# Kernel optimization log

Measured on AMD Instinct MI355X. Metric: run time of the kernel, lower is better.

The kernel has to match this reference:

```python
import jax, jax.numpy as jnp
import numpy as np

GRID = 385  # (W+1) = (H+1) = (D+1) corners of a 384^3 voxel grid


def setup_inputs() -> dict:
    key = jax.random.key(0)
    occ = jax.random.uniform(key, (GRID, GRID, GRID), dtype=jnp.float32)
    return {"occ": occ}


def reference(occ):
    # Occupancy connectivity loss: sum over axis-aligned neighbor pairs of
    # |occ_i - occ_j| (each pair counted once via the 3 forward directions).
    lx = jnp.sum(jnp.abs(occ[1:, :, :] - occ[:-1, :, :]))
    ly = jnp.sum(jnp.abs(occ[:, 1:, :] - occ[:, :-1, :]))
    lz = jnp.sum(jnp.abs(occ[:, :, 1:] - occ[:, :, :-1]))
    return lx + ly + lz
```

## Files before the change

kernel.cpp:

```cpp
#include <hip/hip_runtime.h>


constexpr int          G     = 385;
constexpr int          PLANE = G * G;
constexpr long long    NTOT  = (long long)G * PLANE;
constexpr int          N4    = (int)((NTOT + 3) / 4);

#define TPB    256
#define BLOCKS 2048

__global__ __launch_bounds__(TPB) void occ_conn_partial(
    const float* __restrict__ a, float* __restrict__ ws)
{
    float s = 0.f;
    const int stride = BLOCKS * TPB;
    for (int i = blockIdx.x * TPB + threadIdx.x; i < N4; i += stride) {
        const long long p0 = (long long)i * 4;
        if (p0 + 4 < NTOT) {
            const float4 v4 = *(const float4*)(a + p0);
            const float v[4] = {v4.x, v4.y, v4.z, v4.w};
            const float vnext = a[p0 + 4];
            #pragma unroll
            for (int e = 0; e < 4; ++e) {
                const unsigned p = (unsigned)p0 + (unsigned)e;
                const unsigned x = p / (unsigned)PLANE;
                const unsigned r = p - x * (unsigned)PLANE;
                const unsigned y = r / (unsigned)G;
                const unsigned z = r - y * (unsigned)G;
                const float v0 = v[e];
                if (z < (unsigned)(G - 1)) {
                    const float zn = (e < 3) ? v[e + 1] : vnext;
                    s += fabsf(zn - v0);
                }
                if (y < (unsigned)(G - 1)) s += fabsf(a[p + G] - v0);
                if (x < (unsigned)(G - 1)) s += fabsf(a[p + PLANE] - v0);
            }
        } else {
            #pragma unroll
            for (int e = 0; e < 4; ++e) {
                const long long pl = p0 + e;
                if (pl >= NTOT) break;
                const unsigned p = (unsigned)pl;
                const unsigned x = p / (unsigned)PLANE;
                const unsigned r = p - x * (unsigned)PLANE;
                const unsigned y = r / (unsigned)G;
                const unsigned z = r - y * (unsigned)G;
                const float v0 = a[p];
                if (z < (unsigned)(G - 1)) s += fabsf(a[p + 1]     - v0);
                if (y < (unsigned)(G - 1)) s += fabsf(a[p + G]     - v0);
                if (x < (unsigned)(G - 1)) s += fabsf(a[p + PLANE] - v0);
            }
        }
    }

    #pragma unroll
    for (int off = 32; off > 0; off >>= 1) s += __shfl_down(s, off, 64);

    __shared__ float ls[TPB / 64];
    const int lane = threadIdx.x & 63;
    const int wid  = threadIdx.x >> 6;
    if (lane == 0) ls[wid] = s;
    __syncthreads();
    if (threadIdx.x == 0) {
        float t = 0.f;
        #pragma unroll
        for (int w = 0; w < TPB / 64; ++w) t += ls[w];
        ws[blockIdx.x] = t;
    }
}

__global__ __launch_bounds__(256) void occ_conn_final(
    const float* __restrict__ ws, float* __restrict__ out)
{
    float s = 0.f;
    for (int i = threadIdx.x; i < BLOCKS; i += 256) s += ws[i];
    #pragma unroll
    for (int off = 32; off > 0; off >>= 1) s += __shfl_down(s, off, 64);
    __shared__ float ls[4];
    const int lane = threadIdx.x & 63;
    const int wid  = threadIdx.x >> 6;
    if (lane == 0) ls[wid] = s;
    __syncthreads();
    if (threadIdx.x == 0) out[0] = ls[0] + ls[1] + ls[2] + ls[3];
}

extern "C" void kernel_launch(void* const* d_in, const int* in_sizes, int n_in,
                              void* d_out, int out_size, void* d_ws, size_t ws_size,
                              hipStream_t stream)
{
    const float* a   = (const float*)d_in[0];
    float*       out = (float*)d_out;
    float*       ws  = (float*)d_ws;

    occ_conn_partial<<<BLOCKS, TPB, 0, stream>>>(a, ws);
    occ_conn_final<<<1, 256, 0, stream>>>(ws, out);
}
```

Before: 373.8 us.

## Compute all neighbor diffs unconditionally and subtract boundary wrap terms separately

The main pass now computes the z, y and x differences for every element of the first 384 x-planes without per-element index division or boundary branches. It processes 8 elements per thread with vector loads, and the work is split into 8 slabs. A separate set of fixup blocks subtracts the spurious wrap-around terms at row and plane boundaries and handles the last x-plane. This removes the integer divides and divergent branches from the hot loop. In exchange, the result now relies on boundary terms cancelling exactly, so float rounding may differ slightly, and the y/x neighbor loads are unaligned.

```diff
diff --git a/kernel.cpp b/kernel.cpp
--- a/kernel.cpp
+++ b/kernel.cpp
@@ -1,55 +1,79 @@
 #include <hip/hip_runtime.h>
 
 
-constexpr int          G     = 385;
-constexpr int          PLANE = G * G;
-constexpr long long    NTOT  = (long long)G * PLANE;
-constexpr int          N4    = (int)((NTOT + 3) / 4);
+constexpr int      G      = 385;
+constexpr int      PLANE  = G * G;
+constexpr unsigned NTOT   = 57066625u;
+constexpr unsigned NA     = 384u * PLANE;
+constexpr unsigned SLAB   = NA / 8;
+constexpr unsigned SLAB8  = SLAB / 8;
+constexpr unsigned NROWB  = 147840u;
+constexpr unsigned NYB    = 147840u;
 
-#define TPB    256
-#define BLOCKS 2048
+#define TPB        256
+#define FIX_BLOCKS 64
+#define SUB_BLOCKS 248
+#define MAIN_BLOCKS (SUB_BLOCKS * 8)
+#define ALL_BLOCKS  (FIX_BLOCKS + MAIN_BLOCKS)
 
-__global__ __launch_bounds__(TPB) void occ_conn_partial(
+typedef float f4v __attribute__((ext_vector_type(4)));
+typedef f4v f4u __attribute__((aligned(4)));
+
+static __device__ __forceinline__ f4v ld4a(const float* p) { return *(const f4v*)p; }
+static __device__ __forceinline__ f4v ld4u(const float* p) { return *(const f4u*)p; }
+
+__global__ __launch_bounds__(TPB) void occ_conn_main(
     const float* __restrict__ a, float* __restrict__ ws)
 {
     float s = 0.f;
-    const int stride = BLOCKS * TPB;
-    for (int i = blockIdx.x * TPB + threadIdx.x; i < N4; i += stride) {
-        const long long p0 = (long long)i * 4;
-        if (p0 + 4 < NTOT) {
-            const float4 v4 = *(const float4*)(a + p0);
-            const float v[4] = {v4.x, v4.y, v4.z, v4.w};
-            const float vnext = a[p0 + 4];
-            #pragma unroll
-            for (int e = 0; e < 4; ++e) {
-                const unsigned p = (unsigned)p0 + (unsigned)e;
-                const unsigned x = p / (unsigned)PLANE;
-                const unsigned r = p - x * (unsigned)PLANE;
-                const unsigned y = r / (unsigned)G;
-                const unsigned z = r - y * (unsigned)G;
-                const float v0 = v[e];
-                if (z < (unsigned)(G - 1)) {
-                    const float zn = (e < 3) ? v[e + 1] : vnext;
-                    s += fabsf(zn - v0);
-                }
-                if (y < (unsigned)(G - 1)) s += fabsf(a[p + G] - v0);
-                if (x < (unsigned)(G - 1)) s += fabsf(a[p + PLANE] - v0);
-            }
-        } else {
-            #pragma unroll
-            for (int e = 0; e < 4; ++e) {
-                const long long pl = p0 + e;
-                if (pl >= NTOT) break;
-                const unsigned p = (unsigned)pl;
-                const unsigned x = p / (unsigned)PLANE;
-                const unsigned r = p - x * (unsigned)PLANE;
-                const unsigned y = r / (unsigned)G;
-                const unsigned z = r - y * (unsigned)G;
-                const float v0 = a[p];
-                if (z < (unsigned)(G - 1)) s += fabsf(a[p + 1]     - v0);
-                if (y < (unsigned)(G - 1)) s += fabsf(a[p + G]     - v0);
-                if (x < (unsigned)(G - 1)) s += fabsf(a[p + PLANE] - v0);
-            }
+    const int bid = blockIdx.x;
+
+    if (bid < FIX_BLOCKS) {
+        const unsigned ft = (unsigned)bid * TPB + threadIdx.x;
+        const unsigned NF = FIX_BLOCKS * TPB;
+
+        for (unsigned r = ft; r < NROWB; r += NF) {
+            const unsigned p = r * (unsigned)G + 384u;
+            s -= fabsf(a[p + 1] - a[p]);
+        }
+        for (unsigned j = ft; j < NYB; j += NF) {
+            const unsigned x = j / (unsigned)G;
+            const unsigned z = j - x * (unsigned)G;
+            const unsigned q = x * (unsigned)PLANE + 384u * (unsigned)G + z;
+            s -= fabsf(a[q + G] - a[q]);
+        }
+        for (unsigned j = ft; j < (unsigned)PLANE; j += NF) {
+            const unsigned y = j / (unsigned)G;
+            const unsigned z = j - y * (unsigned)G;
+            const unsigned p = NA + j;
+            if (z < 384u) s += fabsf(a[p + 1] - a[p]);
+            if (y < 384u) s += fabsf(a[p + G] - a[p]);
+        }
+    } else {
+        const int mid  = bid - FIX_BLOCKS;
+        const unsigned slab = (unsigned)(mid & 7);
+        const unsigned sub  = (unsigned)(mid >> 3);
+        const unsigned base = slab * SLAB;
+
+        for (unsigned it = sub * TPB + threadIdx.x; it < SLAB8; it += SUB_BLOCKS * TPB) {
+            const unsigned p = base + it * 8u;
+            const f4v f0 = ld4a(a + p);
+            const f4v f1 = ld4a(a + p + 4);
+            const f4v g0 = ld4u(a + p + G);
+            const f4v g1 = ld4u(a + p + G + 4);
+            const f4v h0 = ld4u(a + p + PLANE);
+            const f4v h1 = ld4u(a + p + PLANE + 4);
+            const float fn = a[p + 8];
+
+            s += fabsf(f0.y - f0.x) + fabsf(f0.z - f0.y) + fabsf(f0.w - f0.z)
+               + fabsf(f1.x - f0.w) + fabsf(f1.y - f1.x) + fabsf(f1.z - f1.y)
+               + fabsf(f1.w - f1.z) + fabsf(fn   - f1.w);
+            s += fabsf(g0.x - f0.x) + fabsf(g0.y - f0.y) + fabsf(g0.z - f0.z)
+               + fabsf(g0.w - f0.w) + fabsf(g1.x - f1.x) + fabsf(g1.y - f1.y)
+               + fabsf(g1.z - f1.z) + fabsf(g1.w - f1.w);
+            s += fabsf(h0.x - f0.x) + fabsf(h0.y - f0.y) + fabsf(h0.z - f0.z)
+               + fabsf(h0.w - f0.w) + fabsf(h1.x - f1.x) + fabsf(h1.y - f1.y)
+               + fabsf(h1.z - f1.z) + fabsf(h1.w - f1.w);
         }
     }
 
@@ -73,7 +97,7 @@
     const float* __restrict__ ws, float* __restrict__ out)
 {
     float s = 0.f;
-    for (int i = threadIdx.x; i < BLOCKS; i += 256) s += ws[i];
+    for (int i = threadIdx.x; i < ALL_BLOCKS; i += 256) s += ws[i];
     #pragma unroll
     for (int off = 32; off > 0; off >>= 1) s += __shfl_down(s, off, 64);
     __shared__ float ls[4];
@@ -92,6 +116,6 @@
     float*       out = (float*)d_out;
     float*       ws  = (float*)d_ws;
 
-    occ_conn_partial<<<BLOCKS, TPB, 0, stream>>>(a, ws);
+    occ_conn_main<<<ALL_BLOCKS, TPB, 0, stream>>>(a, ws);
     occ_conn_final<<<1, 256, 0, stream>>>(ws, out);
 }
```

Measured after the change: 325.4 us. -12.9%, faster.

## Tile grid into z-y slabs marching along x with shared-memory halo reuse

Applied to the files above, without the earlier changes.

Replaces the flat grid-stride loop, which did per-element div/mod and three scattered global loads, with 2D tiles (16 y-rows by 64 z-columns) that march along x. Each plane slice is staged in double-buffered LDS with a halo, and the x-neighbor difference is taken from registers holding the previous plane. The y=384 and z=384 boundary faces are handled by eight separate fixup blocks. The aim is to read each element from DRAM roughly once and drop the index arithmetic, at the cost of one __syncthreads per plane, 4-byte-aligned unaligned vector loads, and more intricate boundary handling.

```diff
diff --git a/kernel.cpp b/kernel.cpp
--- a/kernel.cpp
+++ b/kernel.cpp
@@ -1,55 +1,96 @@
 #include <hip/hip_runtime.h>
 
 
-constexpr int          G     = 385;
-constexpr int          PLANE = G * G;
-constexpr long long    NTOT  = (long long)G * PLANE;
-constexpr int          N4    = (int)((NTOT + 3) / 4);
+constexpr int G     = 385;
+constexpr int PLANE = G * G;
+constexpr int ZT = 6, YT = 24, XC = 16;
+constexpr int XP = 384 / XC;
 
-#define TPB    256
-#define BLOCKS 2048
+#define TPB   256
+#define FIXB  8
+#define TILES (ZT * YT * XC)
+#define ALLB  (TILES + FIXB)
 
-__global__ __launch_bounds__(TPB) void occ_conn_partial(
+typedef float f4v __attribute__((ext_vector_type(4)));
+typedef f4v f4u __attribute__((aligned(4)));
+static __device__ __forceinline__ f4v ld4(const float* p) { return *(const f4u*)p; }
+
+__global__ __launch_bounds__(TPB) void occ_conn_main(
     const float* __restrict__ a, float* __restrict__ ws)
 {
     float s = 0.f;
-    const int stride = BLOCKS * TPB;
-    for (int i = blockIdx.x * TPB + threadIdx.x; i < N4; i += stride) {
-        const long long p0 = (long long)i * 4;
-        if (p0 + 4 < NTOT) {
-            const float4 v4 = *(const float4*)(a + p0);
-            const float v[4] = {v4.x, v4.y, v4.z, v4.w};
-            const float vnext = a[p0 + 4];
-            #pragma unroll
-            for (int e = 0; e < 4; ++e) {
-                const unsigned p = (unsigned)p0 + (unsigned)e;
-                const unsigned x = p / (unsigned)PLANE;
-                const unsigned r = p - x * (unsigned)PLANE;
-                const unsigned y = r / (unsigned)G;
-                const unsigned z = r - y * (unsigned)G;
-                const float v0 = v[e];
-                if (z < (unsigned)(G - 1)) {
-                    const float zn = (e < 3) ? v[e + 1] : vnext;
-                    s += fabsf(zn - v0);
-                }
-                if (y < (unsigned)(G - 1)) s += fabsf(a[p + G] - v0);
-                if (x < (unsigned)(G - 1)) s += fabsf(a[p + PLANE] - v0);
+    const int bid = blockIdx.x;
+
+    __shared__ float T[2][17][68];
+
+    if (bid < FIXB) {
+        const unsigned ft = (unsigned)bid * TPB + threadIdx.x;
+        const unsigned NF = FIXB * TPB;
+
+        for (unsigned j = ft; j < 385u * 384u; j += NF) {
+            const unsigned x = j / 384u, z = j - x * 384u;
+            const unsigned p = x * (unsigned)PLANE + 384u * (unsigned)G + z;
+            s += fabsf(a[p + 1] - a[p]);
+        }
+        for (unsigned j = ft; j < 385u * 384u; j += NF) {
+            const unsigned x = j / 384u, y = j - x * 384u;
+            const unsigned p = x * (unsigned)PLANE + y * (unsigned)G + 384u;
+            s += fabsf(a[p + G] - a[p]);
+        }
+        for (unsigned j = ft; j < 384u * 385u; j += NF) {
+            const unsigned x = j / 385u, z = j - x * 385u;
+            const unsigned p = x * (unsigned)PLANE + 384u * (unsigned)G + z;
+            s += fabsf(a[p + PLANE] - a[p]);
+        }
+        for (unsigned j = ft; j < 384u * 384u; j += NF) {
+            const unsigned x = j / 384u, y = j - x * 384u;
+            const unsigned p = x * (unsigned)PLANE + y * (unsigned)G + 384u;
+            s += fabsf(a[p + PLANE] - a[p]);
+        }
+    } else {
+        int t = bid - FIXB;
+        const int bc = t & (XC - 1); t >>= 4;
+        const int by = t % YT;
+        const int bz = t / YT;
+        const int tz = threadIdx.x & 15;
+        const int ty = threadIdx.x >> 4;
+        const int P0 = bc * XP, P1 = P0 + XP;
+        const bool last = (bc == XC - 1);
+
+        const float* pm  = a + (size_t)P0 * PLANE + (size_t)(by * 16 + ty) * G + (bz * 64 + tz * 4);
+        const float* ph  = a + (size_t)P0 * PLANE + (size_t)(by * 16 + 16) * G + (bz * 64 + tz * 4);
+        const float* pc  = a + (size_t)P0 * PLANE + (size_t)(by * 16 + tz) * G + (bz * 64 + 64);
+        const float* pc2 = a + (size_t)P0 * PLANE + (size_t)(by * 16 + 16) * G + (bz * 64 + 64);
+
+        f4v prev;
+        for (int x = P0; x <= P1; ++x) {
+            const int par = x & 1;
+            const f4v cur = ld4(pm);
+            *(f4v*)&T[par][ty][tz * 4] = cur;
+            if (ty == 0)             *(f4v*)&T[par][16][tz * 4] = ld4(ph);
+            if (ty == 1)             T[par][tz][64] = *pc;
+            if (ty == 2 && tz == 0)  T[par][16][64] = *pc2;
+            __syncthreads();
+
+            if (x < P1 || last) {
+                const float v0 = T[par][ty][tz * 4 + 0];
+                const float v1 = T[par][ty][tz * 4 + 1];
+                const float v2 = T[par][ty][tz * 4 + 2];
+                const float v3 = T[par][ty][tz * 4 + 3];
+                const float v4 = T[par][ty][tz * 4 + 4];
+                const float u0 = T[par][ty + 1][tz * 4 + 0];
+                const float u1 = T[par][ty + 1][tz * 4 + 1];
+                const float u2 = T[par][ty + 1][tz * 4 + 2];
+                const float u3 = T[par][ty + 1][tz * 4 + 3];
+                s += fabsf(v1 - v0) + fabsf(v2 - v1) + fabsf(v3 - v2) + fabsf(v4 - v3);
+                s += fabsf(u0 - v0) + fabsf(u1 - v1) + fabsf(u2 - v2) + fabsf(u3 - v3);
             }
-        } else {
-            #pragma unroll
-            for (int e = 0; e < 4; ++e) {
-                const long long pl = p0 + e;
-                if (pl >= NTOT) break;
-                const unsigned p = (unsigned)pl;
-                const unsigned x = p / (unsigned)PLANE;
-                const unsigned r = p - x * (unsigned)PLANE;
-                const unsigned y = r / (unsigned)G;
-                const unsigned z = r - y * (unsigned)G;
-                const float v0 = a[p];
-                if (z < (unsigned)(G - 1)) s += fabsf(a[p + 1]     - v0);
-                if (y < (unsigned)(G - 1)) s += fabsf(a[p + G]     - v0);
-                if (x < (unsigned)(G - 1)) s += fabsf(a[p + PLANE] - v0);
+            if (x > P0) {
+                s += fabsf(cur.x - prev.x) + fabsf(cur.y - prev.y)
+                   + fabsf(cur.z - prev.z) + fabsf(cur.w - prev.w);
             }
+            prev = cur;
+            pm += PLANE; ph += PLANE; pc += PLANE; pc2 += PLANE;
         }
     }
 
@@ -62,10 +103,10 @@
     if (lane == 0) ls[wid] = s;
     __syncthreads();
     if (threadIdx.x == 0) {
-        float t = 0.f;
+        float tsum = 0.f;
         #pragma unroll
-        for (int w = 0; w < TPB / 64; ++w) t += ls[w];
-        ws[blockIdx.x] = t;
+        for (int w = 0; w < TPB / 64; ++w) tsum += ls[w];
+        ws[blockIdx.x] = tsum;
     }
 }
 
@@ -73,7 +114,7 @@
     const float* __restrict__ ws, float* __restrict__ out)
 {
     float s = 0.f;
-    for (int i = threadIdx.x; i < BLOCKS; i += 256) s += ws[i];
+    for (int i = threadIdx.x; i < ALLB; i += 256) s += ws[i];
     #pragma unroll
     for (int off = 32; off > 0; off >>= 1) s += __shfl_down(s, off, 64);
     __shared__ float ls[4];
@@ -92,6 +133,6 @@
     float*       out = (float*)d_out;
     float*       ws  = (float*)d_ws;
 
-    occ_conn_partial<<<BLOCKS, TPB, 0, stream>>>(a, ws);
+    occ_conn_main<<<ALLB, TPB, 0, stream>>>(a, ws);
     occ_conn_final<<<1, 256, 0, stream>>>(ws, out);
 }
```

After: 402.8 us. +7.8%, slower.

## Tile grid into 3D blocks staged in double-buffered shared memory

Applied to the files above, without the earlier changes.

Replaces the flat grid-stride loop, which reloaded y and x neighbours from global memory for every element, with a 3D tiling. Each block covers a 128z by 32y tile and walks 6 x-planes (plus one halo plane), staging each plane plus its halo in double-buffered LDS with aligned float4 loads. The x-neighbour difference comes from the previous plane's buffer, so each element is read from HBM roughly once. Edge cases are handled per tile, which adds control-flow complexity and some halo reloads across x-chunks.

```diff
diff --git a/kernel.cpp b/kernel.cpp
--- a/kernel.cpp
+++ b/kernel.cpp
@@ -1,71 +1,145 @@
 #include <hip/hip_runtime.h>
 
 
-constexpr int          G     = 385;
-constexpr int          PLANE = G * G;
-constexpr long long    NTOT  = (long long)G * PLANE;
-constexpr int          N4    = (int)((NTOT + 3) / 4);
+constexpr int G     = 385;
+constexpr int PLANE = G * G;
 
-#define TPB    256
-#define BLOCKS 2048
+#define TPB  256
+#define ZT   3
+#define YT   12
+#define XC   64
+#define NBLK (ZT * YT * XC)
+#define S    148
 
-__global__ __launch_bounds__(TPB) void occ_conn_partial(
+typedef float f4v __attribute__((ext_vector_type(4)));
+static __device__ __forceinline__ f4v ld4(const float* p) { return *(const f4v*)p; }
+
+__global__ __launch_bounds__(TPB) void occ_conn_main(
     const float* __restrict__ a, float* __restrict__ ws)
 {
+    __shared__ float T[2][33][S];
     float s = 0.f;
-    const int stride = BLOCKS * TPB;
-    for (int i = blockIdx.x * TPB + threadIdx.x; i < N4; i += stride) {
-        const long long p0 = (long long)i * 4;
-        if (p0 + 4 < NTOT) {
-            const float4 v4 = *(const float4*)(a + p0);
-            const float v[4] = {v4.x, v4.y, v4.z, v4.w};
-            const float vnext = a[p0 + 4];
-            #pragma unroll
-            for (int e = 0; e < 4; ++e) {
-                const unsigned p = (unsigned)p0 + (unsigned)e;
-                const unsigned x = p / (unsigned)PLANE;
-                const unsigned r = p - x * (unsigned)PLANE;
-                const unsigned y = r / (unsigned)G;
-                const unsigned z = r - y * (unsigned)G;
-                const float v0 = v[e];
-                if (z < (unsigned)(G - 1)) {
-                    const float zn = (e < 3) ? v[e + 1] : vnext;
-                    s += fabsf(zn - v0);
-                }
-                if (y < (unsigned)(G - 1)) s += fabsf(a[p + G] - v0);
-                if (x < (unsigned)(G - 1)) s += fabsf(a[p + PLANE] - v0);
-            }
-        } else {
-            #pragma unroll
-            for (int e = 0; e < 4; ++e) {
-                const long long pl = p0 + e;
-                if (pl >= NTOT) break;
-                const unsigned p = (unsigned)pl;
-                const unsigned x = p / (unsigned)PLANE;
-                const unsigned r = p - x * (unsigned)PLANE;
-                const unsigned y = r / (unsigned)G;
-                const unsigned z = r - y * (unsigned)G;
-                const float v0 = a[p];
-                if (z < (unsigned)(G - 1)) s += fabsf(a[p + 1]     - v0);
-                if (y < (unsigned)(G - 1)) s += fabsf(a[p + G]     - v0);
-                if (x < (unsigned)(G - 1)) s += fabsf(a[p + PLANE] - v0);
+
+    const int tz = threadIdx.x & 31;
+    const int ty = threadIdx.x >> 5;
+
+    int t = blockIdx.x;
+    const int bc = t % XC;  t /= XC;
+    const int by = t % YT;  t /= YT;
+    const int bz = t;
+    const unsigned gy0 = by * 32u;
+    const unsigned gz0 = bz * 128u;
+    const int  P0    = bc * 6;
+    const bool lastc = (bc == XC - 1);
+    const bool ey    = (by == YT - 1);
+    const bool ez    = (bz == ZT - 1);
+
+    f4v m0, m1, m2, m3, h;
+
+    for (int tt = 0; tt <= 7; ++tt) {
+        const int x = P0 + tt;
+
+        if (tt <= 6) {
+            const unsigned base = (unsigned)x * (unsigned)PLANE + gy0 * (unsigned)G + gz0;
+            const unsigned W0 = base + (unsigned)ty * (unsigned)G;
+            const unsigned W1 = W0 +  8u * (unsigned)G;
+            const unsigned W2 = W0 + 16u * (unsigned)G;
+            const unsigned W3 = W0 + 24u * (unsigned)G;
+            m0 = ld4(a + (W0 - (W0 & 3u)) + 4u * (unsigned)tz);
+            m1 = ld4(a + (W1 - (W1 & 3u)) + 4u * (unsigned)tz);
+            m2 = ld4(a + (W2 - (W2 & 3u)) + 4u * (unsigned)tz);
+            m3 = ld4(a + (W3 - (W3 & 3u)) + 4u * (unsigned)tz);
+            if (ty == 0) {
+                const unsigned W32 = base + 32u * (unsigned)G;
+                h = ld4(a + (W32 - (W32 & 3u)) + 4u * (unsigned)tz);
+            } else if (ty == 1) {
+                const unsigned Wr = base + (unsigned)tz * (unsigned)G;
+                h = ld4(a + (Wr - (Wr & 3u)) + 128u);
+            } else if (ty == 2 && tz == 0) {
+                const unsigned W32 = base + 32u * (unsigned)G;
+                h = ld4(a + (W32 - (W32 & 3u)) + 128u);
             }
         }
+
+        if (tt >= 1) {
+            const int xc = x - 1;
+            const float (*C)[S]  = T[(tt - 1) & 1];
+            const float (*Pv)[S] = T[tt & 1];
+            const bool zy = (tt <= 6) || (lastc && tt == 7);
+            const bool xd = (tt >= 2);
+
+            #pragma unroll
+            for (int rr = 0; rr < 4; ++rr) {
+                const int r = ty + 8 * rr;
+                const unsigned phi  = (unsigned)(xc + (int)gy0 + r) & 3u;
+                const unsigned phin = (phi + 1u) & 3u;
+                const unsigned phip = (phi + 3u) & 3u;
+                #pragma unroll
+                for (int j = 0; j < 4; ++j) {
+                    const int zl = tz + 32 * j;
+                    const float v = C[r][phi + zl];
+                    if (zy) {
+                        s += fabsf(C[r][phi + zl + 1] - v);
+                        s += fabsf(C[r + 1][phin + zl] - v);
+                    }
+                    if (xd) s += fabsf(v - Pv[r][phip + zl]);
+                }
+            }
+
+            if (ez && ty == 4) {
+                const int r = tz;
+                const unsigned phi  = (unsigned)(xc + (int)gy0 + r) & 3u;
+                const unsigned phin = (phi + 1u) & 3u;
+                const unsigned phip = (phi + 3u) & 3u;
+                const float v = C[r][phi + 128];
+                if (zy) s += fabsf(C[r + 1][phin + 128] - v);
+                if (xd) s += fabsf(v - Pv[r][phip + 128]);
+            }
+            if (ey && ty == 5) {
+                const unsigned phi  = (unsigned)(xc + (int)gy0 + 32) & 3u;
+                const unsigned phip = (phi + 3u) & 3u;
+                #pragma unroll
+                for (int j = 0; j < 4; ++j) {
+                    const int zl = tz + 32 * j;
+                    const float v = C[32][phi + zl];
+                    if (zy) s += fabsf(C[32][phi + zl + 1] - v);
+                    if (xd) s += fabsf(v - Pv[32][phip + zl]);
+                }
+            }
+            if (ey && ez && ty == 6 && tz == 0 && xd) {
+                const unsigned phi  = (unsigned)(xc + (int)gy0 + 32) & 3u;
+                const unsigned phip = (phi + 3u) & 3u;
+                s += fabsf(C[32][phi + 128] - Pv[32][phip + 128]);
+            }
+        }
+
+        __syncthreads();
+
+        if (tt <= 6) {
+            float (*B)[S] = T[tt & 1];
+            *(f4v*)&B[ty +  0][4 * tz] = m0;
+            *(f4v*)&B[ty +  8][4 * tz] = m1;
+            *(f4v*)&B[ty + 16][4 * tz] = m2;
+            *(f4v*)&B[ty + 24][4 * tz] = m3;
+            if      (ty == 0)            *(f4v*)&B[32][4 * tz] = h;
+            else if (ty == 1)            *(f4v*)&B[tz][128]    = h;
+            else if (ty == 2 && tz == 0) *(f4v*)&B[32][128]    = h;
+        }
+        __syncthreads();
     }
 
     #pragma unroll
     for (int off = 32; off > 0; off >>= 1) s += __shfl_down(s, off, 64);
-
     __shared__ float ls[TPB / 64];
     const int lane = threadIdx.x & 63;
     const int wid  = threadIdx.x >> 6;
     if (lane == 0) ls[wid] = s;
     __syncthreads();
     if (threadIdx.x == 0) {
-        float t = 0.f;
+        float tsum = 0.f;
         #pragma unroll
-        for (int w = 0; w < TPB / 64; ++w) t += ls[w];
-        ws[blockIdx.x] = t;
+        for (int w = 0; w < TPB / 64; ++w) tsum += ls[w];
+        ws[blockIdx.x] = tsum;
     }
 }
 
@@ -73,7 +147,7 @@
     const float* __restrict__ ws, float* __restrict__ out)
 {
     float s = 0.f;
-    for (int i = threadIdx.x; i < BLOCKS; i += 256) s += ws[i];
+    for (int i = threadIdx.x; i < NBLK; i += 256) s += ws[i];
     #pragma unroll
     for (int off = 32; off > 0; off >>= 1) s += __shfl_down(s, off, 64);
     __shared__ float ls[4];
@@ -92,6 +166,6 @@
     float*       out = (float*)d_out;
     float*       ws  = (float*)d_ws;
 
-    occ_conn_partial<<<BLOCKS, TPB, 0, stream>>>(a, ws);
+    occ_conn_main<<<NBLK, TPB, 0, stream>>>(a, ws);
     occ_conn_final<<<1, 256, 0, stream>>>(ws, out);
 }
```

Measured after the change: 316.8 us. 1.18x faster.
